# Kernel tuning notes

Measured on AMD Instinct MI355X. Metric: run time of the kernel, lower is better.

## Reference

```python
import jax, jax.numpy as jnp
import numpy as np

N_NODES = 100000
N_EDGES = 1600000
IN_DIM, HID, OUT = 128, 64, 64
KERNEL = 5
PAD = (KERNEL - 1) // 2


def setup_inputs() -> dict:
    key = jax.random.key(0)
    ks = jax.random.split(key, 12)
    s = lambda fan_in: 1.0 / np.sqrt(fan_in)
    return {
        "x": jax.random.normal(ks[0], (N_NODES, IN_DIM), jnp.float32),
        "edge_index": jax.random.randint(ks[1], (2, N_EDGES), 0, N_NODES, jnp.int32),
        "W0": jax.random.normal(ks[2], (IN_DIM, HID), jnp.float32) * s(IN_DIM),
        "b0": jnp.zeros((HID,), jnp.float32),
        "W1": jax.random.normal(ks[3], (HID, HID), jnp.float32) * s(HID),
        "b1": jnp.zeros((HID,), jnp.float32),
        "W2": jax.random.normal(ks[4], (HID, OUT), jnp.float32) * s(HID),
        "b2": jnp.zeros((OUT,), jnp.float32),
        "Wp": jax.random.normal(ks[5], (OUT, 1), jnp.float32) * s(OUT),
        "bp": jnp.zeros((1,), jnp.float32),
        "conv1_w": jax.random.normal(ks[6], (OUT, OUT, KERNEL), jnp.float32) * s(OUT * KERNEL),
        "conv1_b": jnp.zeros((OUT,), jnp.float32),
        "conv2_w": jax.random.normal(ks[7], (OUT, OUT, KERNEL), jnp.float32) * s(OUT * KERNEL),
        "conv2_b": jnp.zeros((OUT,), jnp.float32),
        "lin_w": jax.random.normal(ks[8], (2 * OUT, OUT), jnp.float32) * s(2 * OUT),
        "lin_b": jnp.zeros((OUT,), jnp.float32),
    }


def gcn_conv(h, W, b, src, dst, n):
    """PyG GCNConv: x @ W, add self-loops, D^-1/2 (A+I) D^-1/2 aggregation, + bias."""
    h = h @ W  # [N, out]
    loop = jnp.arange(n, dtype=src.dtype)
    srcl = jnp.concatenate([src, loop])
    dstl = jnp.concatenate([dst, loop])
    deg = jax.ops.segment_sum(jnp.ones_like(dstl, dtype=h.dtype), dstl, num_segments=n)
    dinv = jnp.where(deg > 0, jax.lax.rsqrt(deg), 0.0)
    norm = dinv[srcl] * dinv[dstl]  # [E+N]
    out = jax.ops.segment_sum(h[srcl] * norm[:, None], dstl, num_segments=n)
    return out + b


def conv1d(x, w, b):
    # x: [1, C, N], w: [Cout, Cin, K]
    y = jax.lax.conv_general_dilated(x, w, window_strides=(1,), padding=[(PAD, PAD)],
                                     dimension_numbers=("NCH", "OIH", "NCH"))
    return y + b[None, :, None]


def reference(x, edge_index, W0, b0, W1, b1, W2, b2, Wp, bp,
              conv1_w, conv1_b, conv2_w, conv2_b, lin_w, lin_b):
    n = x.shape[0]
    src, dst = edge_index[0], edge_index[1]
    # eval mode: dropout layers are identity
    h = jax.nn.relu(gcn_conv(x, W0, b0, src, dst, n))
    h = jax.nn.relu(gcn_conv(h, W1, b1, src, dst, n))
    h1 = gcn_conv(h, W2, b2, src, dst, n)  # [N, OUT]
    g_score = h1 @ Wp + bp  # [N, 1]
    sorted_idx = jnp.argsort(g_score[:, 0])  # ascending, as torch.sort
    inverse_idx = jnp.argsort(sorted_idx)
    sorted_x = g_score[sorted_idx] * h1[sorted_idx]  # [N, OUT]
    sorted_x = sorted_x.T[None]  # [1, OUT, N]
    sorted_x = jax.nn.relu(conv1d(sorted_x, conv1_w, conv1_b))
    sorted_x = conv1d(sorted_x, conv2_w, conv2_b)
    sorted_x = sorted_x[0].T  # [N, OUT]
    h2 = sorted_x[inverse_idx]  # un-sort back to node order
    out = jnp.concatenate([h1, h2], axis=1) @ lin_w + lin_b  # [N, OUT]
    return out
```

## Files before the change

kernel.cpp:

```cpp
#include <hip/hip_runtime.h>

#define NN 100000
#define NE 1600000
#define SORT_M 131072
#define NB_SCAN 98
#define TS 8192

__global__ void zero_counts(int* c) {
    int i = blockIdx.x * blockDim.x + threadIdx.x;
    if (i < NN) c[i] = 0;
}

__global__ void count_dst(const int* __restrict__ dst, int* c) {
    int e = blockIdx.x * blockDim.x + threadIdx.x;
    if (e < NE) atomicAdd(&c[dst[e]], 1);
}

__global__ void scan_p1(const int* __restrict__ c, int* __restrict__ bsums) {
    __shared__ int red[256];
    int b = blockIdx.x, t = threadIdx.x;
    int s = 0;
    for (int i = t; i < 1024; i += 256) {
        int idx = b * 1024 + i;
        s += (idx < NN) ? c[idx] : 0;
    }
    red[t] = s; __syncthreads();
    for (int o = 128; o; o >>= 1) {
        if (t < o) red[t] += red[t + o];
        __syncthreads();
    }
    if (t == 0) bsums[b] = red[0];
}

__global__ void scan_p2(int* bsums) {
    __shared__ int tmp[128];
    int t = threadIdx.x;
    int v = (t < NB_SCAN) ? bsums[t] : 0;
    tmp[t] = v; __syncthreads();
    for (int o = 1; o < 128; o <<= 1) {
        int add = (t >= o) ? tmp[t - o] : 0;
        __syncthreads();
        tmp[t] += add;
        __syncthreads();
    }
    if (t < NB_SCAN) bsums[t] = tmp[t] - v;
}

__global__ void scan_p3(const int* __restrict__ c, const int* __restrict__ bsums,
                        int* __restrict__ offs, int* __restrict__ cursor,
                        float* __restrict__ dinv) {
    __shared__ int thr[256];
    int b = blockIdx.x, t = threadIdx.x;
    int base = b * 1024 + t * 4;
    int cv[4];
#pragma unroll
    for (int j = 0; j < 4; j++) cv[j] = (base + j < NN) ? c[base + j] : 0;
    int s = cv[0] + cv[1] + cv[2] + cv[3];
    thr[t] = s; __syncthreads();
    for (int o = 1; o < 256; o <<= 1) {
        int add = (t >= o) ? thr[t - o] : 0;
        __syncthreads();
        thr[t] += add;
        __syncthreads();
    }
    int ex = thr[t] - s + bsums[b];
#pragma unroll
    for (int j = 0; j < 4; j++) {
        if (base + j < NN) {
            offs[base + j] = ex;
            cursor[base + j] = ex;
            dinv[base + j] = rsqrtf((float)(cv[j] + 1));
            ex += cv[j];
        }
    }
}

__global__ void csr_scatter(const int* __restrict__ src, const int* __restrict__ dst,
                            const float* __restrict__ dinv, int* cursor,
                            int2* __restrict__ csr) {
    int e = blockIdx.x * blockDim.x + threadIdx.x;
    if (e >= NE) return;
    int s = src[e], d = dst[e];
    int p = atomicAdd(&cursor[d], 1);
    float nrm = dinv[s] * dinv[d];
    csr[p] = make_int2(s, __float_as_int(nrm));
}

__device__ inline void swz_w(const float* __restrict__ W, float4* __restrict__ o, int idx) {
    int k4 = idx >> 6, co = idx & 63;
    o[idx] = make_float4(W[(4 * k4 + 0) * 64 + co], W[(4 * k4 + 1) * 64 + co],
                         W[(4 * k4 + 2) * 64 + co], W[(4 * k4 + 3) * 64 + co]);
}

__device__ inline void swz_c(const float* __restrict__ w, float4* __restrict__ o, int idx) {
    int co = idx & 63, j = (idx >> 6) & 15, k = idx >> 10;
    int b = co * 320 + k;
    o[idx] = make_float4(w[b + (4 * j + 0) * 5], w[b + (4 * j + 1) * 5],
                         w[b + (4 * j + 2) * 5], w[b + (4 * j + 3) * 5]);
}

__global__ void swizzle_all(const float* W0, const float* W1, const float* W2,
                            const float* lw, const float* c1w, const float* c2w,
                            float4* w0sw, float4* w1sw, float4* w2sw,
                            float4* linsw, float4* c1sw, float4* c2sw) {
    int idx = blockIdx.x * blockDim.x + threadIdx.x;
    if (idx < 2048)        swz_w(W0, w0sw, idx);
    else if (idx < 3072)   swz_w(W1, w1sw, idx - 2048);
    else if (idx < 4096)   swz_w(W2, w2sw, idx - 3072);
    else if (idx < 6144)   swz_w(lw, linsw, idx - 4096);
    else if (idx < 11264)  swz_c(c1w, c1sw, idx - 6144);
    else if (idx < 16384)  swz_c(c2w, c2sw, idx - 11264);
}

template <int K, bool RELU>
__global__ __launch_bounds__(256) void gemm64r(const float* __restrict__ X,
                                               const float4* __restrict__ Wsw,
                                               float* __restrict__ Y, int n) {
    constexpr int KV = K / 4;
    constexpr int SH = (KV == 32) ? 5 : 4;
    __shared__ float4 xs[64][KV];
    int tid = threadIdx.x;
    int r0 = blockIdx.x * 64;
    for (int idx = tid; idx < 64 * KV; idx += 256) {
        int r = idx >> SH, k4 = idx & (KV - 1);
        int row = r0 + r;
        float4 v = make_float4(0.f, 0.f, 0.f, 0.f);
        if (row < n) v = *reinterpret_cast<const float4*>(X + (size_t)row * K + 4 * k4);
        if (RELU) {
            v.x = fmaxf(v.x, 0.f); v.y = fmaxf(v.y, 0.f);
            v.z = fmaxf(v.z, 0.f); v.w = fmaxf(v.w, 0.f);
        }
        xs[r][k4] = v;
    }
    __syncthreads();
    int co2 = tid & 31, rg = tid >> 5;
    int c0 = 2 * co2;
    float acc0[8], acc1[8];
#pragma unroll
    for (int i = 0; i < 8; i++) { acc0[i] = 0.f; acc1[i] = 0.f; }
    for (int k4 = 0; k4 < KV; k4++) {
        float4 wa = Wsw[k4 * 64 + c0];
        float4 wb = Wsw[k4 * 64 + c0 + 1];
#pragma unroll
        for (int i = 0; i < 8; i++) {
            float4 xv = xs[rg * 8 + i][k4];
            acc0[i] += xv.x * wa.x + xv.y * wa.y + xv.z * wa.z + xv.w * wa.w;
            acc1[i] += xv.x * wb.x + xv.y * wb.y + xv.z * wb.z + xv.w * wb.w;
        }
    }
#pragma unroll
    for (int i = 0; i < 8; i++) {
        int row = r0 + rg * 8 + i;
        if (row < n)
            *reinterpret_cast<float2*>(Y + (size_t)row * 64 + c0) = make_float2(acc0[i], acc1[i]);
    }
}

template <int SCORE>
__global__ __launch_bounds__(256) void agg_pull(const float* __restrict__ H,
                                                const int* __restrict__ offs,
                                                const int* __restrict__ counts,
                                                const int2* __restrict__ csr,
                                                const float* __restrict__ dinv,
                                                const float* __restrict__ bias,
                                                float* __restrict__ Y,
                                                const float* __restrict__ Wp,
                                                const float* __restrict__ bp,
                                                float* __restrict__ sc,
                                                unsigned* __restrict__ keys,
                                                int* __restrict__ vals) {
    int lane = threadIdx.x & 63;
    int node = blockIdx.x * 4 + (threadIdx.x >> 6);
    if (node >= NN) return;
    float dv = dinv[node];
    float acc = H[(size_t)node * 64 + lane] * dv * dv + bias[lane];
    int off = offs[node], cnt = counts[node];
    int i = 0;
    for (; i + 7 < cnt; i += 8) {
        int2 p0 = csr[off + i];
        int2 p1 = csr[off + i + 1];
        int2 p2 = csr[off + i + 2];
        int2 p3 = csr[off + i + 3];
        int2 p4 = csr[off + i + 4];
        int2 p5 = csr[off + i + 5];
        int2 p6 = csr[off + i + 6];
        int2 p7 = csr[off + i + 7];
        float h0 = H[(size_t)p0.x * 64 + lane];
        float h1 = H[(size_t)p1.x * 64 + lane];
        float h2 = H[(size_t)p2.x * 64 + lane];
        float h3 = H[(size_t)p3.x * 64 + lane];
        float h4 = H[(size_t)p4.x * 64 + lane];
        float h5 = H[(size_t)p5.x * 64 + lane];
        float h6 = H[(size_t)p6.x * 64 + lane];
        float h7 = H[(size_t)p7.x * 64 + lane];
        acc += h0 * __int_as_float(p0.y) + h1 * __int_as_float(p1.y) +
               h2 * __int_as_float(p2.y) + h3 * __int_as_float(p3.y) +
               h4 * __int_as_float(p4.y) + h5 * __int_as_float(p5.y) +
               h6 * __int_as_float(p6.y) + h7 * __int_as_float(p7.y);
    }
    for (; i < cnt; i++) {
        int2 p = csr[off + i];
        acc += H[(size_t)p.x * 64 + lane] * __int_as_float(p.y);
    }
    Y[(size_t)node * 64 + lane] = acc;
    if (SCORE) {
        float v = acc * Wp[lane];
        for (int o = 32; o; o >>= 1) v += __shfl_down(v, o, 64);
        if (lane == 0) {
            float s = v + bp[0];
            sc[node] = s;
            unsigned u = __float_as_uint(s);
            u = (u & 0x80000000u) ? ~u : (u | 0x80000000u);
            keys[node] = u;
            vals[node] = node;
        }
    }
}

__global__ __launch_bounds__(1024) void bitonic_local_sort8k(unsigned* key, int* val) {
    __shared__ unsigned sk[TS];
    __shared__ int sv[TS];
    int t = threadIdx.x;
    int base = blockIdx.x * TS;
    for (int i = t; i < TS; i += 1024) {
        if (base + i < NN) { sk[i] = key[base + i]; sv[i] = val[base + i]; }
        else               { sk[i] = 0xFFFFFFFFu;  sv[i] = 0x7FFFFFFF; }
    }
    for (int k = 2; k <= TS; k <<= 1) {
        for (int j = k >> 1; j > 0; j >>= 1) {
            __syncthreads();
            for (int c = t; c < TS / 2; c += 1024) {
                int i = 2 * c - (c & (j - 1));
                bool up = (((base + i) & k) == 0);
                unsigned a = sk[i], b = sk[i + j];
                if ((a > b) == up) {
                    sk[i] = b; sk[i + j] = a;
                    int tv = sv[i]; sv[i] = sv[i + j]; sv[i + j] = tv;
                }
            }
        }
    }
    __syncthreads();
    for (int i = t; i < TS; i += 1024) { key[base + i] = sk[i]; val[base + i] = sv[i]; }
}

__global__ void bitonic_global(unsigned* key, int* val, int j, int k) {
    int i = blockIdx.x * blockDim.x + threadIdx.x;
    int ixj = i ^ j;
    if (ixj > i) {
        bool up = ((i & k) == 0);
        unsigned a = key[i], b = key[ixj];
        if ((a > b) == up) {
            key[i] = b; key[ixj] = a;
            int tv = val[i]; val[i] = val[ixj]; val[ixj] = tv;
        }
    }
}

__global__ __launch_bounds__(1024) void bitonic_local_merge8k(unsigned* key, int* val, int k) {
    __shared__ unsigned sk[TS];
    __shared__ int sv[TS];
    int t = threadIdx.x;
    int base = blockIdx.x * TS;
    for (int i = t; i < TS; i += 1024) { sk[i] = key[base + i]; sv[i] = val[base + i]; }
    for (int j = TS / 2; j > 0; j >>= 1) {
        __syncthreads();
        for (int c = t; c < TS / 2; c += 1024) {
            int i = 2 * c - (c & (j - 1));
            bool up = (((base + i) & k) == 0);
            unsigned a = sk[i], b = sk[i + j];
            if ((a > b) == up) {
                sk[i] = b; sk[i + j] = a;
                int tv = sv[i]; sv[i] = sv[i + j]; sv[i + j] = tv;
            }
        }
    }
    __syncthreads();
    for (int i = t; i < TS; i += 1024) { key[base + i] = sk[i]; val[base + i] = sv[i]; }
}

template <bool GATHER>
__global__ __launch_bounds__(256) void conv1d_k(const float* __restrict__ X,
                                                const int* __restrict__ vals,
                                                const float* __restrict__ sc,
                                                const float4* __restrict__ cw,
                                                const float* __restrict__ bias,
                                                float* __restrict__ Y, int relu,
                                                int* __restrict__ inv) {
    __shared__ float4 xs[68][16];
    int tid = threadIdx.x;
    int r0 = blockIdx.x * 64;
    for (int idx = tid; idx < 68 * 16; idx += 256) {
        int r = idx >> 4, k4 = idx & 15;
        int row = r0 + r - 2;
        float4 v = make_float4(0.f, 0.f, 0.f, 0.f);
        if (row >= 0 && row < NN) {
            if (GATHER) {
                int vs = vals[row];
                float s = sc[vs];
                v = *reinterpret_cast<const float4*>(X + (size_t)vs * 64 + 4 * k4);
                v.x *= s; v.y *= s; v.z *= s; v.w *= s;
                if (k4 == 0) inv[vs] = row;
            } else {
                v = *reinterpret_cast<const float4*>(X + (size_t)row * 64 + 4 * k4);
            }
        }
        xs[r][k4] = v;
    }
    __syncthreads();
    int co2 = tid & 31, rg = tid >> 5;
    int c0 = 2 * co2;
    float acc0[8], acc1[8];
#pragma unroll
    for (int i = 0; i < 8; i++) { acc0[i] = 0.f; acc1[i] = 0.f; }
    for (int j = 0; j < 16; j++) {
        float4 xv[12];
#pragma unroll
        for (int t2 = 0; t2 < 12; t2++) xv[t2] = xs[rg * 8 + t2][j];
#pragma unroll
        for (int k = 0; k < 5; k++) {
            float4 wa = cw[(k * 16 + j) * 64 + c0];
            float4 wb = cw[(k * 16 + j) * 64 + c0 + 1];
#pragma unroll
            for (int i = 0; i < 8; i++) {
                float4 x4 = xv[i + k];
                acc0[i] += x4.x * wa.x + x4.y * wa.y + x4.z * wa.z + x4.w * wa.w;
                acc1[i] += x4.x * wb.x + x4.y * wb.y + x4.z * wb.z + x4.w * wb.w;
            }
        }
    }
    float b0v = bias[c0], b1v = bias[c0 + 1];
#pragma unroll
    for (int i = 0; i < 8; i++) {
        int row = r0 + rg * 8 + i;
        if (row < NN) {
            float o0 = acc0[i] + b0v, o1 = acc1[i] + b1v;
            if (relu) { o0 = fmaxf(o0, 0.f); o1 = fmaxf(o1, 0.f); }
            *reinterpret_cast<float2*>(Y + (size_t)row * 64 + c0) = make_float2(o0, o1);
        }
    }
}

__global__ __launch_bounds__(256) void final_k(const float* __restrict__ C,
                                               const float* __restrict__ H2,
                                               const int* __restrict__ inv,
                                               const float4* __restrict__ linsw,
                                               const float* __restrict__ lb,
                                               float* __restrict__ Yout) {
    __shared__ float4 xs[64][32];
    int tid = threadIdx.x;
    int r0 = blockIdx.x * 64;
    for (int idx = tid; idx < 64 * 32; idx += 256) {
        int r = idx >> 5, k4 = idx & 31;
        int row = r0 + r;
        float4 v = make_float4(0.f, 0.f, 0.f, 0.f);
        if (row < NN) {
            if (k4 < 16) v = *reinterpret_cast<const float4*>(C + (size_t)row * 64 + 4 * k4);
            else v = *reinterpret_cast<const float4*>(H2 + (size_t)inv[row] * 64 + 4 * (k4 - 16));
        }
        xs[r][k4] = v;
    }
    __syncthreads();
    int co2 = tid & 31, rg = tid >> 5;
    int c0 = 2 * co2;
    float acc0[8], acc1[8];
#pragma unroll
    for (int i = 0; i < 8; i++) { acc0[i] = 0.f; acc1[i] = 0.f; }
    for (int k4 = 0; k4 < 32; k4++) {
        float4 wa = linsw[k4 * 64 + c0];
        float4 wb = linsw[k4 * 64 + c0 + 1];
#pragma unroll
        for (int i = 0; i < 8; i++) {
            float4 xv = xs[rg * 8 + i][k4];
            acc0[i] += xv.x * wa.x + xv.y * wa.y + xv.z * wa.z + xv.w * wa.w;
            acc1[i] += xv.x * wb.x + xv.y * wb.y + xv.z * wb.z + xv.w * wb.w;
        }
    }
    float b0v = lb[c0], b1v = lb[c0 + 1];
#pragma unroll
    for (int i = 0; i < 8; i++) {
        int row = r0 + rg * 8 + i;
        if (row < NN)
            *reinterpret_cast<float2*>(Yout + (size_t)row * 64 + c0) =
                make_float2(acc0[i] + b0v, acc1[i] + b1v);
    }
}

extern "C" void kernel_launch(void* const* d_in, const int* in_sizes, int n_in,
                              void* d_out, int out_size, void* d_ws, size_t ws_size,
                              hipStream_t stream) {
    const float* x   = (const float*)d_in[0];
    const int*   ei  = (const int*)d_in[1];
    const float* W0  = (const float*)d_in[2];
    const float* b0  = (const float*)d_in[3];
    const float* W1  = (const float*)d_in[4];
    const float* b1  = (const float*)d_in[5];
    const float* W2  = (const float*)d_in[6];
    const float* b2  = (const float*)d_in[7];
    const float* Wp  = (const float*)d_in[8];
    const float* bp  = (const float*)d_in[9];
    const float* c1w = (const float*)d_in[10];
    const float* c1b = (const float*)d_in[11];
    const float* c2w = (const float*)d_in[12];
    const float* c2b = (const float*)d_in[13];
    const float* lw  = (const float*)d_in[14];
    const float* lb  = (const float*)d_in[15];
    const int* src = ei;
    const int* dst = ei + NE;

    float* A     = (float*)d_ws;
    float* B     = A + (size_t)NN * 64;
    float* dinv  = B + (size_t)NN * 64;
    float* score = dinv + NN;
    unsigned* keys = (unsigned*)(score + NN);
    int* vals    = (int*)(keys + SORT_M);
    int* inv     = vals + SORT_M;
    int* counts  = inv + NN;
    int* offs    = counts + NN;
    int* cursor  = offs + NN;
    int* bsums   = cursor + NN;
    int2* csr    = (int2*)(bsums + 128);
    float4* w0sw  = (float4*)(csr + NE);
    float4* w1sw  = w0sw + 2048;
    float4* w2sw  = w1sw + 1024;
    float4* linsw = w2sw + 1024;
    float4* c1sw  = linsw + 2048;
    float4* c2sw  = c1sw + 5120;
    float* Cb = (float*)d_out;

    const int GR64 = (NN + 63) / 64;
    const int GN4 = (NN + 3) / 4;

    zero_counts<<<(NN + 255) / 256, 256, 0, stream>>>(counts);
    count_dst<<<(NE + 255) / 256, 256, 0, stream>>>(dst, counts);
    scan_p1<<<NB_SCAN, 256, 0, stream>>>(counts, bsums);
    scan_p2<<<1, 128, 0, stream>>>(bsums);
    scan_p3<<<NB_SCAN, 256, 0, stream>>>(counts, bsums, offs, cursor, dinv);
    csr_scatter<<<(NE + 255) / 256, 256, 0, stream>>>(src, dst, dinv, cursor, csr);

    swizzle_all<<<64, 256, 0, stream>>>(W0, W1, W2, lw, c1w, c2w,
                                        w0sw, w1sw, w2sw, linsw, c1sw, c2sw);

    gemm64r<128, false><<<GR64, 256, 0, stream>>>(x, w0sw, A, NN);
    agg_pull<0><<<GN4, 256, 0, stream>>>(A, offs, counts, csr, dinv, b0, B,
                                         nullptr, nullptr, nullptr, nullptr, nullptr);
    gemm64r<64, true><<<GR64, 256, 0, stream>>>(B, w1sw, A, NN);
    agg_pull<0><<<GN4, 256, 0, stream>>>(A, offs, counts, csr, dinv, b1, B,
                                         nullptr, nullptr, nullptr, nullptr, nullptr);
    gemm64r<64, true><<<GR64, 256, 0, stream>>>(B, w2sw, A, NN);
    agg_pull<1><<<GN4, 256, 0, stream>>>(A, offs, counts, csr, dinv, b2, Cb,
                                         Wp, bp, score, keys, vals);

    bitonic_local_sort8k<<<SORT_M / TS, 1024, 0, stream>>>(keys, vals);
    for (int k = 2 * TS; k <= SORT_M; k <<= 1) {
        for (int j = k >> 1; j >= TS; j >>= 1)
            bitonic_global<<<SORT_M / 256, 256, 0, stream>>>(keys, vals, j, k);
        bitonic_local_merge8k<<<SORT_M / TS, 1024, 0, stream>>>(keys, vals, k);
    }

    conv1d_k<true><<<GR64, 256, 0, stream>>>(Cb, vals, score, c1sw, c1b, B, 1, inv);
    conv1d_k<false><<<GR64, 256, 0, stream>>>(B, nullptr, nullptr, c2sw, c2b, A, 0, nullptr);

    final_k<<<GR64, 256, 0, stream>>>(Cb, A, inv, linsw, lb, (float*)d_out);
}
```

Measured before the change: 948.1 us.

## Fold GCN normalization into GEMM epilogue, store src-only CSR, scatter in dst-range passes

The symmetric normalization dinv[s]*dinv[d] is factored out: the GEMM epilogue pre-scales each row by dinv[row], and aggregation multiplies the summed neighbor rows by dinv[node] once. The CSR therefore stores only int source indices instead of int2 (index, weight), halving the edge-stream bytes read in the three aggregation passes. The CSR build is split into four passes by destination range (d>>15) so atomic cursor updates and writes stay localized. The cost is four full reads of the edge arrays during CSR construction and a slightly different floating-point summation order.

```diff
diff --git a/kernel.cpp b/kernel.cpp
--- a/kernel.cpp
+++ b/kernel.cpp
@@ -75,15 +75,14 @@
     }
 }
 
-__global__ void csr_scatter(const int* __restrict__ src, const int* __restrict__ dst,
-                            const float* __restrict__ dinv, int* cursor,
-                            int2* __restrict__ csr) {
+__global__ void csr_scatter_p(const int* __restrict__ src, const int* __restrict__ dst,
+                              int* cursor, int* __restrict__ csr, int pass) {
     int e = blockIdx.x * blockDim.x + threadIdx.x;
     if (e >= NE) return;
-    int s = src[e], d = dst[e];
+    int d = dst[e];
+    if ((d >> 15) != pass) return;
     int p = atomicAdd(&cursor[d], 1);
-    float nrm = dinv[s] * dinv[d];
-    csr[p] = make_int2(s, __float_as_int(nrm));
+    csr[p] = src[e];
 }
 
 __device__ inline void swz_w(const float* __restrict__ W, float4* __restrict__ o, int idx) {
@@ -115,6 +114,7 @@
 template <int K, bool RELU>
 __global__ __launch_bounds__(256) void gemm64r(const float* __restrict__ X,
                                                const float4* __restrict__ Wsw,
+                                               const float* __restrict__ dinv,
                                                float* __restrict__ Y, int n) {
     constexpr int KV = K / 4;
     constexpr int SH = (KV == 32) ? 5 : 4;
@@ -151,8 +151,11 @@
 #pragma unroll
     for (int i = 0; i < 8; i++) {
         int row = r0 + rg * 8 + i;
-        if (row < n)
-            *reinterpret_cast<float2*>(Y + (size_t)row * 64 + c0) = make_float2(acc0[i], acc1[i]);
+        if (row < n) {
+            float dv = dinv[row];
+            *reinterpret_cast<float2*>(Y + (size_t)row * 64 + c0) =
+                make_float2(acc0[i] * dv, acc1[i] * dv);
+        }
     }
 }
 
@@ -160,7 +163,7 @@
 __global__ __launch_bounds__(256) void agg_pull(const float* __restrict__ H,
                                                 const int* __restrict__ offs,
                                                 const int* __restrict__ counts,
-                                                const int2* __restrict__ csr,
+                                                const int* __restrict__ csr,
                                                 const float* __restrict__ dinv,
                                                 const float* __restrict__ bias,
                                                 float* __restrict__ Y,
@@ -173,39 +176,36 @@
     int node = blockIdx.x * 4 + (threadIdx.x >> 6);
     if (node >= NN) return;
     float dv = dinv[node];
-    float acc = H[(size_t)node * 64 + lane] * dv * dv + bias[lane];
+    float acc = H[(size_t)node * 64 + lane];
     int off = offs[node], cnt = counts[node];
     int i = 0;
     for (; i + 7 < cnt; i += 8) {
-        int2 p0 = csr[off + i];
-        int2 p1 = csr[off + i + 1];
-        int2 p2 = csr[off + i + 2];
-        int2 p3 = csr[off + i + 3];
-        int2 p4 = csr[off + i + 4];
-        int2 p5 = csr[off + i + 5];
-        int2 p6 = csr[off + i + 6];
-        int2 p7 = csr[off + i + 7];
-        float h0 = H[(size_t)p0.x * 64 + lane];
-        float h1 = H[(size_t)p1.x * 64 + lane];
-        float h2 = H[(size_t)p2.x * 64 + lane];
-        float h3 = H[(size_t)p3.x * 64 + lane];
-        float h4 = H[(size_t)p4.x * 64 + lane];
-        float h5 = H[(size_t)p5.x * 64 + lane];
-        float h6 = H[(size_t)p6.x * 64 + lane];
-        float h7 = H[(size_t)p7.x * 64 + lane];
-        acc += h0 * __int_as_float(p0.y) + h1 * __int_as_float(p1.y) +
-               h2 * __int_as_float(p2.y) + h3 * __int_as_float(p3.y) +
-               h4 * __int_as_float(p4.y) + h5 * __int_as_float(p5.y) +
-               h6 * __int_as_float(p6.y) + h7 * __int_as_float(p7.y);
+        int p0 = csr[off + i];
+        int p1 = csr[off + i + 1];
+        int p2 = csr[off + i + 2];
+        int p3 = csr[off + i + 3];
+        int p4 = csr[off + i + 4];
+        int p5 = csr[off + i + 5];
+        int p6 = csr[off + i + 6];
+        int p7 = csr[off + i + 7];
+        float h0 = H[(size_t)p0 * 64 + lane];
+        float h1 = H[(size_t)p1 * 64 + lane];
+        float h2 = H[(size_t)p2 * 64 + lane];
+        float h3 = H[(size_t)p3 * 64 + lane];
+        float h4 = H[(size_t)p4 * 64 + lane];
+        float h5 = H[(size_t)p5 * 64 + lane];
+        float h6 = H[(size_t)p6 * 64 + lane];
+        float h7 = H[(size_t)p7 * 64 + lane];
+        acc += ((h0 + h1) + (h2 + h3)) + ((h4 + h5) + (h6 + h7));
     }
     for (; i < cnt; i++) {
-        int2 p = csr[off + i];
-        acc += H[(size_t)p.x * 64 + lane] * __int_as_float(p.y);
-    }
-    Y[(size_t)node * 64 + lane] = acc;
+        acc += H[(size_t)csr[off + i] * 64 + lane];
+    }
+    float o = acc * dv + bias[lane];
+    Y[(size_t)node * 64 + lane] = o;
     if (SCORE) {
-        float v = acc * Wp[lane];
-        for (int o = 32; o; o >>= 1) v += __shfl_down(v, o, 64);
+        float v = o * Wp[lane];
+        for (int of = 32; of; of >>= 1) v += __shfl_down(v, of, 64);
         if (lane == 0) {
             float s = v + bp[0];
             sc[node] = s;
@@ -419,7 +419,7 @@
     int* offs    = counts + NN;
     int* cursor  = offs + NN;
     int* bsums   = cursor + NN;
-    int2* csr    = (int2*)(bsums + 128);
+    int* csr     = bsums + 128;
     float4* w0sw  = (float4*)(csr + NE);
     float4* w1sw  = w0sw + 2048;
     float4* w2sw  = w1sw + 1024;
@@ -430,24 +430,26 @@
 
     const int GR64 = (NN + 63) / 64;
     const int GN4 = (NN + 3) / 4;
+    const int GE = (NE + 255) / 256;
 
     zero_counts<<<(NN + 255) / 256, 256, 0, stream>>>(counts);
-    count_dst<<<(NE + 255) / 256, 256, 0, stream>>>(dst, counts);
+    count_dst<<<GE, 256, 0, stream>>>(dst, counts);
     scan_p1<<<NB_SCAN, 256, 0, stream>>>(counts, bsums);
     scan_p2<<<1, 128, 0, stream>>>(bsums);
     scan_p3<<<NB_SCAN, 256, 0, stream>>>(counts, bsums, offs, cursor, dinv);
-    csr_scatter<<<(NE + 255) / 256, 256, 0, stream>>>(src, dst, dinv, cursor, csr);
+    for (int pass = 0; pass < 4; pass++)
+        csr_scatter_p<<<GE, 256, 0, stream>>>(src, dst, cursor, csr, pass);
 
     swizzle_all<<<64, 256, 0, stream>>>(W0, W1, W2, lw, c1w, c2w,
                                         w0sw, w1sw, w2sw, linsw, c1sw, c2sw);
 
-    gemm64r<128, false><<<GR64, 256, 0, stream>>>(x, w0sw, A, NN);
+    gemm64r<128, false><<<GR64, 256, 0, stream>>>(x, w0sw, dinv, A, NN);
     agg_pull<0><<<GN4, 256, 0, stream>>>(A, offs, counts, csr, dinv, b0, B,
                                          nullptr, nullptr, nullptr, nullptr, nullptr);
-    gemm64r<64, true><<<GR64, 256, 0, stream>>>(B, w1sw, A, NN);
+    gemm64r<64, true><<<GR64, 256, 0, stream>>>(B, w1sw, dinv, A, NN);
     agg_pull<0><<<GN4, 256, 0, stream>>>(A, offs, counts, csr, dinv, b1, B,
                                          nullptr, nullptr, nullptr, nullptr, nullptr);
-    gemm64r<64, true><<<GR64, 256, 0, stream>>>(B, w2sw, A, NN);
+    gemm64r<64, true><<<GR64, 256, 0, stream>>>(B, w2sw, dinv, A, NN);
     agg_pull<1><<<GN4, 256, 0, stream>>>(A, offs, counts, csr, dinv, b2, Cb,
                                          Wp, bp, score, keys, vals);
 
```

After: 972.8 us. 2.6% more time.
